# Optimization experiments

Measured on AMD Instinct MI355X. Metric: run time of the kernel, lower is better.

Reference implementation:

```python
import jax, jax.numpy as jnp
import numpy as np
from jax import lax

EPS = 1e-5
DN = ('NCHW', 'OIHW', 'NCHW')

def _sign(v):
    # (v >= 0) * 2 - 1
    return jnp.where(v >= 0, 1.0, -1.0).astype(v.dtype)

def _conv(x, w, b):
    y = lax.conv_general_dilated(x, w, (1, 1), 'VALID', dimension_numbers=DN)
    return y + b[None, :, None, None]

def _bn(x):
    # BatchNorm2d(affine=False), training mode: biased batch stats over (N,H,W)
    m = jnp.mean(x, axis=(0, 2, 3), keepdims=True)
    v = jnp.var(x, axis=(0, 2, 3), keepdims=True)
    return (x - m) * lax.rsqrt(v + EPS)

def setup_inputs() -> dict:
    key = jax.random.key(0)
    ks = jax.random.split(key, 9)
    f = jnp.float32
    B = 8192
    x = jax.random.normal(ks[0], (B, 1, 28, 28), dtype=f)
    # conv params, clipped to [-1, 1] as in clip_weights()
    w1 = jnp.clip(jax.random.normal(ks[1], (32, 1, 9, 9), dtype=f) * 0.1, -1, 1)
    b1 = jnp.clip(jax.random.normal(ks[2], (32,), dtype=f) * 0.1, -1, 1)
    w2 = jnp.clip(jax.random.normal(ks[3], (16, 32, 9, 9), dtype=f) * 0.1, -1, 1)
    b2 = jnp.clip(jax.random.normal(ks[4], (16,), dtype=f) * 0.1, -1, 1)
    w3 = jnp.clip(jax.random.normal(ks[5], (8, 16, 9, 9), dtype=f) * 0.1, -1, 1)
    b3 = jnp.clip(jax.random.normal(ks[6], (8,), dtype=f) * 0.1, -1, 1)
    wl = jnp.clip(jax.random.normal(ks[7], (10, 8, 4, 4), dtype=f) * 0.1, -1, 1)
    bl = jnp.clip(jax.random.normal(ks[8], (10,), dtype=f) * 0.1, -1, 1)
    return {"x": x, "w1": w1, "b1": b1, "w2": w2, "b2": b2,
            "w3": w3, "b3": b3, "wl": wl, "bl": bl}

def _block(x, w, b, act=True, norm=True, binarized=True):
    if binarized:
        w, b = _sign(w), _sign(b)
    x = _conv(x, w, b)
    if norm:
        x = _bn(x)
    if act:
        x = _sign(x) if binarized else jax.nn.relu(x)
    return x

def reference(x, w1, b1, w2, b2, w3, b3, wl, bl):
    x = _sign(x)                        # binarize input activations
    x = _block(x, w1, b1)               # (B, 32, 20, 20)
    x = _block(x, w2, b2)               # (B, 16, 12, 12)
    x = _block(x, w3, b3)               # (B,  8,  4,  4)
    x = _block(x, wl, bl, act=False, norm=False)  # (B, 10, 1, 1), binarized weights
    return x.reshape(-1, 10)
```

## Files before the change

### kernel.cpp

```cpp
#include <hip/hip_runtime.h>
#include <stdint.h>

#define BATCH 8192

#define OFF_W1R3   0
#define OFF_W2P    384
#define OFF_W3P    6144
#define OFF_WLB    9600
#define OFF_SBL    9760
#define OFF_TTOT   9856
#define OFF_S3     10184
#define OFF_S2PART 10496
#define OFF_Z2     76800
#define OFF_Z3     37825792

__global__ __launch_bounds__(256) void k1_pack_tsum(const float* __restrict__ x,
                                                    const float* __restrict__ w1,
                                                    const float* __restrict__ w2,
                                                    const float* __restrict__ w3,
                                                    const float* __restrict__ wl,
                                                    const float* __restrict__ bl,
                                                    uint8_t* __restrict__ ws) {
  int* Ttot = (int*)(ws + OFF_TTOT);
  const int tid = threadIdx.x;

  if (blockIdx.x == 0) {
    uint32_t* W1R3 = (uint32_t*)(ws + OFF_W1R3);
    uint32_t* W2P  = (uint32_t*)(ws + OFF_W2P);
    uint32_t* W3P  = (uint32_t*)(ws + OFF_W3P);
    uint64_t* WLB  = (uint64_t*)(ws + OFF_WLB);
    float*    SBL  = (float*)(ws + OFF_SBL);
    for (int e = tid; e < 96; e += 256) {
      int oc = e / 3, i = e % 3;
      uint32_t m = 0;
      for (int rr = 0; rr < 3; ++rr)
        for (int kw = 0; kw < 9; ++kw)
          if (w1[oc*81 + (3*i+rr)*9 + kw] < 0.f) m |= 1u << (rr*9 + kw);
      W1R3[e] = m;
    }
    for (int e = tid; e < 648; e += 256) {
      int och = e / 81, k = e % 81;
      int kh = k / 9, kw = k % 9;
      uint32_t m0 = 0, m1 = 0;
      int oc0 = och*2;
      for (int ic = 0; ic < 32; ++ic) {
        if (w2[(oc0*32 + ic)*81 + k] < 0.f)     m0 |= 1u << ic;
        if (w2[((oc0+1)*32 + ic)*81 + k] < 0.f) m1 |= 1u << ic;
      }
      int idx = ((och*9 + kh)*10 + kw)*2;
      W2P[idx] = m0; W2P[idx+1] = m1;
    }
    for (int e = tid; e < 72; e += 256) {
      int idx = (e*10 + 9)*2;
      W2P[idx] = 0; W2P[idx+1] = 0;
    }
    for (int e = tid; e < 648; e += 256) {
      int oc = e / 81, k = e % 81;
      int kh = k / 9, kw = k % 9;
      uint32_t m = 0;
      for (int ic = 0; ic < 16; ++ic)
        if (w3[(oc*16 + ic)*81 + k] < 0.f) m |= 1u << ic;
      W3P[(oc*9 + kh)*12 + kw] = m;
    }
    for (int e = tid; e < 216; e += 256) {
      int row = e / 3, p = e % 3;
      W3P[row*12 + 9 + p] = 0;
    }
    for (int e = tid; e < 20; e += 256) {
      int oc = e >> 1, word = e & 1;
      uint64_t m = 0;
      for (int b = 0; b < 64; ++b)
        if (wl[oc*128 + word*64 + b] < 0.f) m |= 1ull << b;
      WLB[e] = m;
    }
    if (tid < 10) SBL[tid] = (bl[tid] >= 0.f) ? 1.f : -1.f;
  }

  __shared__ uint32_t rowm[896];
  __shared__ int Tacc[81];
  if (tid < 81) Tacc[tid] = 0;
  __syncthreads();

  const int img0 = blockIdx.x * 32;
  #pragma unroll
  for (int it = 0; it < 4; ++it) {
    int R = tid + it*256;
    if (R < 896) {
      int il = R / 28, r = R % 28;
      const float4* xr = (const float4*)(x + (size_t)(img0 + il) * 784 + r * 28);
      uint32_t m = 0;
      #pragma unroll
      for (int j = 0; j < 7; ++j) {
        float4 v = xr[j];
        if (v.x < 0.f) m |= 1u << (j*4+0);
        if (v.y < 0.f) m |= 1u << (j*4+1);
        if (v.z < 0.f) m |= 1u << (j*4+2);
        if (v.w < 0.f) m |= 1u << (j*4+3);
      }
      rowm[R] = m;
    }
  }
  __syncthreads();

  for (int T = tid; T < 288; T += 256) {
    int il = T / 9, kw = T % 9;
    int base = il * 28;
    int n9[9];
    int sum20 = 0;
    #pragma unroll
    for (int r = 0; r < 20; ++r) {
      int n = __popc((rowm[base + r] >> kw) & 0xFFFFFu);
      if (r < 9) n9[r] = n;
      sum20 += n;
    }
    atomicAdd(&Tacc[kw], 400 - 2*sum20);
    #pragma unroll
    for (int kh = 1; kh <= 8; ++kh) {
      int nadd = __popc((rowm[base + kh + 19] >> kw) & 0xFFFFFu);
      sum20 += nadd - n9[kh-1];
      atomicAdd(&Tacc[kh*9 + kw], 400 - 2*sum20);
    }
  }
  __syncthreads();
  if (tid < 81) atomicAdd(&Ttot[tid], Tacc[tid]);
}

#define K2_IMGS 8
__global__ __launch_bounds__(256) void k2_conv12(const float* __restrict__ x,
                                                 uint8_t* __restrict__ ws) {
  const uint32_t* W1R3g = (const uint32_t*)(ws + OFF_W1R3);
  const uint32_t* W2Pg  = (const uint32_t*)(ws + OFF_W2P);
  const int* Ttot = (const int*)(ws + OFF_TTOT);
  int* S2P = (int*)(ws + OFF_S2PART);

  __shared__ uint32_t __attribute__((aligned(16))) rowm[K2_IMGS*28];
  __shared__ uint32_t __attribute__((aligned(16))) w1r3[96];
  __shared__ uint32_t __attribute__((aligned(16))) w2p[1440];
  __shared__ int tlds[81];
  __shared__ int t1s[32];
  __shared__ uint32_t __attribute__((aligned(16))) A1s[K2_IMGS*400];
  __shared__ int s2acc[16];

  const int tid = threadIdx.x;
  const int img0 = blockIdx.x * K2_IMGS;

  for (int e = tid; e < 96; e += 256)   w1r3[e] = W1R3g[e];
  for (int e = tid; e < 1440; e += 256) w2p[e]  = W2Pg[e];
  if (tid < 81) tlds[tid] = Ttot[tid];
  if (tid < 16) s2acc[tid] = 0;
  if (tid < K2_IMGS*28) {
    int il = tid / 28, rr = tid % 28;
    const float4* xr = (const float4*)(x + (size_t)(img0 + il) * 784 + rr * 28);
    uint32_t m = 0;
    #pragma unroll
    for (int j = 0; j < 7; ++j) {
      float4 v = xr[j];
      if (v.x < 0.f) m |= 1u << (j*4+0);
      if (v.y < 0.f) m |= 1u << (j*4+1);
      if (v.z < 0.f) m |= 1u << (j*4+2);
      if (v.w < 0.f) m |= 1u << (j*4+3);
    }
    rowm[tid] = m;
  }
  __syncthreads();

  if (tid < 32) {
    long long S = 0;
    for (int kh = 0; kh < 9; ++kh)
      for (int kw = 0; kw < 9; ++kw) {
        int bit = (w1r3[tid*3 + kh/3] >> ((kh%3)*9 + kw)) & 1;
        S += (long long)(1 - 2*bit) * tlds[kh*9 + kw];
      }
    const long long N1 = (long long)BATCH * 400;
    long long q = S / N1, rr = S % N1;
    long long t = q + (rr > 0 ? 1 : 0);
    if ((t & 1) == 0) t += 1;
    t1s[tid] = (int)t;
  }
  __syncthreads();

  for (int G = tid; G < K2_IMGS*80; G += 256) {
    int il = G / 80, rem = G - il*80;
    int oh = rem >> 2, ow0 = (rem & 3) * 5;
    uint32_t R[9];
    #pragma unroll
    for (int i = 0; i < 9; ++i) R[i] = rowm[il*28 + oh + i];
    uint32_t win[5][3];
    #pragma unroll
    for (int j = 0; j < 5; ++j) {
      int ow = ow0 + j;
      #pragma unroll
      for (int i = 0; i < 3; ++i) {
        uint32_t b0 = (R[3*i]   >> ow) & 0x1FFu;
        uint32_t b1 = (R[3*i+1] >> ow) & 0x1FFu;
        uint32_t b2 = (R[3*i+2] >> ow) & 0x1FFu;
        win[j][i] = b0 | (b1 << 9) | (b2 << 18);
      }
    }
    uint32_t mask[5] = {0,0,0,0,0};
    #pragma unroll
    for (int ocg = 0; ocg < 4; ++ocg) {
      const uint4* wp = (const uint4*)&w1r3[ocg*24];
      uint32_t wr[24];
      #pragma unroll
      for (int q = 0; q < 6; ++q) {
        uint4 v = wp[q];
        wr[q*4+0]=v.x; wr[q*4+1]=v.y; wr[q*4+2]=v.z; wr[q*4+3]=v.w;
      }
      #pragma unroll
      for (int o8 = 0; o8 < 8; ++o8) {
        int oc = ocg*8 + o8;
        int t = t1s[oc];
        #pragma unroll
        for (int j = 0; j < 5; ++j) {
          int mm = __popc(win[j][0] ^ wr[o8*3])
                 + __popc(win[j][1] ^ wr[o8*3+1])
                 + __popc(win[j][2] ^ wr[o8*3+2]);
          mask[j] |= (uint32_t)((81 - 2*mm) < t) << oc;
        }
      }
    }
    #pragma unroll
    for (int j = 0; j < 5; ++j) A1s[il*400 + oh*20 + ow0 + j] = mask[j];
  }
  __syncthreads();

  uint32_t* Z2w = (uint32_t*)(ws + OFF_Z2);
  const int och = tid & 7, oc0 = och << 1;
  int sl0 = 0, sl1 = 0;
  for (int r = 0; r < 3; ++r) {
    int G = tid + r*256;
    int il = G / 96, rem = G - il*96;
    int oy = rem >> 3;
    const uint32_t* A = &A1s[il*400 + oy*20];
    int acc0[12], acc1[12];
    #pragma unroll
    for (int p = 0; p < 12; ++p) { acc0[p] = 0; acc1[p] = 0; }
    for (int kh = 0; kh < 9; ++kh) {
      const uint4* ar = (const uint4*)(A + kh*20);
      uint32_t a[20];
      #pragma unroll
      for (int q = 0; q < 5; ++q) {
        uint4 v = ar[q];
        a[q*4+0]=v.x; a[q*4+1]=v.y; a[q*4+2]=v.z; a[q*4+3]=v.w;
      }
      const uint4* wp4 = (const uint4*)&w2p[(och*9 + kh)*20];
      uint32_t wbuf[20];
      #pragma unroll
      for (int q = 0; q < 5; ++q) {
        uint4 v = wp4[q];
        wbuf[q*4+0]=v.x; wbuf[q*4+1]=v.y; wbuf[q*4+2]=v.z; wbuf[q*4+3]=v.w;
      }
      #pragma unroll
      for (int kw = 0; kw < 9; ++kw) {
        uint32_t w0 = wbuf[2*kw], w1v = wbuf[2*kw+1];
        #pragma unroll
        for (int px = 0; px < 12; ++px) {
          acc0[px] += __popc(a[kw+px] ^ w0);
          acc1[px] += __popc(a[kw+px] ^ w1v);
        }
      }
    }
    size_t wbase = (size_t)(img0+il)*1152 + (size_t)oy*96 + och;
    #pragma unroll
    for (int px = 0; px < 12; ++px) {
      int z0 = 2592 - 2*acc0[px], z1v = 2592 - 2*acc1[px];
      sl0 += z0; sl1 += z1v;
      Z2w[wbase + px*8] = (uint32_t)(uint16_t)(int16_t)z0
                        | ((uint32_t)(uint16_t)(int16_t)z1v << 16);
    }
  }
  atomicAdd(&s2acc[oc0],   sl0);
  atomicAdd(&s2acc[oc0+1], sl1);
  __syncthreads();
  if (tid < 16) S2P[blockIdx.x*16 + tid] = s2acc[tid];
}

__global__ __launch_bounds__(256) void k3_conv3(uint8_t* __restrict__ ws) {
  const int* S2P = (const int*)(ws + OFF_S2PART);
  const uint32_t* W3Pg = (const uint32_t*)(ws + OFF_W3P);
  const uint32_t* Z2w = (const uint32_t*)(ws + OFF_Z2);
  uint32_t* Z3w = (uint32_t*)(ws + OFF_Z3);
  unsigned long long* S3 = (unsigned long long*)(ws + OFF_S3);

  __shared__ uint32_t __attribute__((aligned(16))) w3p[864];
  __shared__ int part[256];
  __shared__ int t2s[16];
  __shared__ uint32_t __attribute__((aligned(16))) A2[32*144];
  __shared__ int s3acc[8];

  const int tid = threadIdx.x;
  const int img0 = blockIdx.x * 32;

  {
    int c = tid & 15, g = tid >> 4;
    int s = 0;
    for (int j = 0; j < 64; ++j) s += S2P[(g + 16*j)*16 + c];
    part[tid] = s;
  }
  for (int e = tid; e < 864; e += 256) w3p[e] = W3Pg[e];
  if (tid < 8) s3acc[tid] = 0;
  __syncthreads();
  if (tid < 16) {
    long long S = 0;
    #pragma unroll
    for (int g = 0; g < 16; ++g) S += (long long)part[g*16 + tid];
    const long long N2 = (long long)BATCH * 144;
    long long q = S / N2, r = S % N2;
    long long t = q + (r > 0 ? 1 : 0);
    if (t & 1) t += 1;
    t2s[tid] = (int)t;
  }
  __syncthreads();

  #pragma unroll
  for (int j = 0; j < 18; ++j) {
    int idx = tid + j*256;
    const uint4* zp = (const uint4*)&Z2w[(size_t)(img0 + idx/144)*1152 + (size_t)(idx%144)*8];
    uint4 v0 = zp[0], v1 = zp[1];
    uint32_t zz[8] = {v0.x,v0.y,v0.z,v0.w, v1.x,v1.y,v1.z,v1.w};
    uint32_t m = 0;
    #pragma unroll
    for (int i = 0; i < 8; ++i) {
      int zlo = (int)(short)(zz[i] & 0xFFFFu);
      int zhi = (int)zz[i] >> 16;
      m |= (uint32_t)(zlo < t2s[2*i])   << (2*i);
      m |= (uint32_t)(zhi < t2s[2*i+1]) << (2*i+1);
    }
    A2[idx] = m;
  }
  __syncthreads();

  const int il = tid >> 3, oc = tid & 7;
  int acc[16];
  #pragma unroll
  for (int i = 0; i < 16; ++i) acc[i] = 0;
  #pragma unroll
  for (int r = 0; r < 12; ++r) {
    const uint4* ar = (const uint4*)&A2[il*144 + r*12];
    uint4 v0 = ar[0], v1 = ar[1], v2 = ar[2];
    uint32_t a[12] = {v0.x,v0.y,v0.z,v0.w, v1.x,v1.y,v1.z,v1.w, v2.x,v2.y,v2.z,v2.w};
    #pragma unroll
    for (int oy = 0; oy < 4; ++oy) {
      if (r - oy >= 0 && r - oy <= 8) {
        int kh = r - oy;
        const uint4* wr = (const uint4*)&w3p[(oc*9 + kh)*12];
        uint4 w0 = wr[0], w1v = wr[1], w2v = wr[2];
        uint32_t w[9] = {w0.x,w0.y,w0.z,w0.w, w1v.x,w1v.y,w1v.z,w1v.w, w2v.x};
        #pragma unroll
        for (int ox = 0; ox < 4; ++ox) {
          int m = 0;
          #pragma unroll
          for (int kw = 0; kw < 9; ++kw) m += __popc(a[ox+kw] ^ w[kw]);
          acc[oy*4+ox] += m;
        }
      }
    }
  }
  int ssum = 0;
  uint32_t packed[8];
  #pragma unroll
  for (int h = 0; h < 8; ++h) {
    int za = 1296 - 2*acc[2*h], zb = 1296 - 2*acc[2*h+1];
    ssum += za + zb;
    packed[h] = (uint32_t)(uint16_t)(int16_t)za | ((uint32_t)(uint16_t)(int16_t)zb << 16);
  }
  uint4* zp = (uint4*)&Z3w[(size_t)(img0 + il)*64 + oc*8];
  zp[0] = make_uint4(packed[0], packed[1], packed[2], packed[3]);
  zp[1] = make_uint4(packed[4], packed[5], packed[6], packed[7]);
  atomicAdd(&s3acc[oc], ssum);
  __syncthreads();
  if (tid < 8)
    atomicAdd(&S3[tid], (unsigned long long)(long long)s3acc[tid]);
}

__global__ __launch_bounds__(256) void k4_final(uint8_t* __restrict__ ws,
                                                float* __restrict__ out) {
  const uint32_t* Z3w = (const uint32_t*)(ws + OFF_Z3);
  const long long* S3 = (const long long*)(ws + OFF_S3);
  const uint64_t* WLBg = (const uint64_t*)(ws + OFF_WLB);
  const float* SBLg = (const float*)(ws + OFF_SBL);
  __shared__ int t3[8];
  __shared__ uint64_t wlb[20];
  __shared__ float sbl[10];
  const int tid = threadIdx.x;
  if (tid < 8) {
    long long S = S3[tid];
    const long long N3 = (long long)BATCH * 16;
    long long q = S / N3, r = S % N3;
    long long t = q + (r > 0 ? 1 : 0);
    if (t & 1) t += 1;
    t3[tid] = (int)t;
  }
  if (tid < 20) wlb[tid] = WLBg[tid];
  if (tid < 10) sbl[tid] = SBLg[tid];
  __syncthreads();
  int img = blockIdx.x * 256 + tid;
  const uint4* zp = (const uint4*)&Z3w[(size_t)img * 64];
  uint32_t zz[64];
  #pragma unroll
  for (int q = 0; q < 16; ++q) {
    uint4 v = zp[q];
    zz[q*4+0]=v.x; zz[q*4+1]=v.y; zz[q*4+2]=v.z; zz[q*4+3]=v.w;
  }
  uint64_t a0 = 0, a1 = 0;
  #pragma unroll
  for (int j = 0; j < 64; ++j) {
    int z = (j & 1) ? ((int)zz[j>>1] >> 16) : (int)(short)(zz[j>>1] & 0xFFFFu);
    a0 |= (uint64_t)(z < t3[j >> 4]) << j;
  }
  #pragma unroll
  for (int j = 0; j < 64; ++j) {
    int z = (j & 1) ? ((int)zz[32 + (j>>1)] >> 16) : (int)(short)(zz[32 + (j>>1)] & 0xFFFFu);
    a1 |= (uint64_t)(z < t3[(64 + j) >> 4]) << j;
  }
  #pragma unroll
  for (int oc = 0; oc < 10; ++oc) {
    int mism = __popcll(a0 ^ wlb[oc*2]) + __popcll(a1 ^ wlb[oc*2 + 1]);
    out[(size_t)img*10 + oc] = (float)(128 - 2*mism) + sbl[oc];
  }
}

extern "C" void kernel_launch(void* const* d_in, const int* in_sizes, int n_in,
                              void* d_out, int out_size, void* d_ws, size_t ws_size,
                              hipStream_t stream) {
  (void)in_sizes; (void)n_in; (void)out_size; (void)ws_size;
  const float* x  = (const float*)d_in[0];
  const float* w1 = (const float*)d_in[1];
  const float* w2 = (const float*)d_in[3];
  const float* w3 = (const float*)d_in[5];
  const float* wl = (const float*)d_in[7];
  const float* bl = (const float*)d_in[8];
  uint8_t* ws = (uint8_t*)d_ws;
  float* out = (float*)d_out;

  hipMemsetAsync(ws + OFF_TTOT, 0, 400, stream);
  k1_pack_tsum<<<256, 256, 0, stream>>>(x, w1, w2, w3, wl, bl, ws);
  k2_conv12<<<1024, 256, 0, stream>>>(x, ws);
  k3_conv3<<<256, 256, 0, stream>>>(ws);
  k4_final<<<32, 256, 0, stream>>>(ws, out);
}
```

Before: 267.8 us.

## Restructure conv2 to one output channel per thread and halve per-block work

The conv2 stage now gives each thread a single output channel instead of a pair. This cuts the accumulator and weight registers, stores fp16-sized halfwords directly, and repacks the conv2 weights per channel with 12-word padded rows. Blocks handle 4 images instead of 8, with twice as many blocks and a launch-bounds occupancy hint. k1 and k4 are also split into more, smaller blocks. The conv1 threshold is precomputed as a popcount bound, and the conv2 partial sums are folded into 256 atomically-accumulated slots that are zeroed by the memset. In exchange, the halfword stores are narrower and weight staging per block is more redundant.

New measurement: 310.6 us. 1.16x slower.

```diff
diff --git a/kernel.cpp b/kernel.cpp
--- a/kernel.cpp
+++ b/kernel.cpp
@@ -5,12 +5,12 @@
 
 #define OFF_W1R3   0
 #define OFF_W2P    384
-#define OFF_W3P    6144
-#define OFF_WLB    9600
-#define OFF_SBL    9760
-#define OFF_TTOT   9856
-#define OFF_S3     10184
-#define OFF_S2PART 10496
+#define OFF_W3P    7296
+#define OFF_WLB    10752
+#define OFF_SBL    10912
+#define OFF_TTOT   10960
+#define OFF_S3     11288
+#define OFF_S2PART 11360
 #define OFF_Z2     76800
 #define OFF_Z3     37825792
 
@@ -38,21 +38,17 @@
           if (w1[oc*81 + (3*i+rr)*9 + kw] < 0.f) m |= 1u << (rr*9 + kw);
       W1R3[e] = m;
     }
-    for (int e = tid; e < 648; e += 256) {
-      int och = e / 81, k = e % 81;
+    for (int e = tid; e < 1296; e += 256) {
+      int oc = e / 81, k = e % 81;
       int kh = k / 9, kw = k % 9;
-      uint32_t m0 = 0, m1 = 0;
-      int oc0 = och*2;
-      for (int ic = 0; ic < 32; ++ic) {
-        if (w2[(oc0*32 + ic)*81 + k] < 0.f)     m0 |= 1u << ic;
-        if (w2[((oc0+1)*32 + ic)*81 + k] < 0.f) m1 |= 1u << ic;
-      }
-      int idx = ((och*9 + kh)*10 + kw)*2;
-      W2P[idx] = m0; W2P[idx+1] = m1;
-    }
-    for (int e = tid; e < 72; e += 256) {
-      int idx = (e*10 + 9)*2;
-      W2P[idx] = 0; W2P[idx+1] = 0;
+      uint32_t m = 0;
+      for (int ic = 0; ic < 32; ++ic)
+        if (w2[(oc*32 + ic)*81 + k] < 0.f) m |= 1u << ic;
+      W2P[(oc*9 + kh)*12 + kw] = m;
+    }
+    for (int e = tid; e < 432; e += 256) {
+      int row = e / 3, p = e % 3;
+      W2P[row*12 + 9 + p] = 0;
     }
     for (int e = tid; e < 648; e += 256) {
       int oc = e / 81, k = e % 81;
@@ -76,16 +72,16 @@
     if (tid < 10) SBL[tid] = (bl[tid] >= 0.f) ? 1.f : -1.f;
   }
 
-  __shared__ uint32_t rowm[896];
+  __shared__ uint32_t rowm[448];
   __shared__ int Tacc[81];
   if (tid < 81) Tacc[tid] = 0;
   __syncthreads();
 
-  const int img0 = blockIdx.x * 32;
-  #pragma unroll
-  for (int it = 0; it < 4; ++it) {
+  const int img0 = blockIdx.x * 16;
+  #pragma unroll
+  for (int it = 0; it < 2; ++it) {
     int R = tid + it*256;
-    if (R < 896) {
+    if (R < 448) {
       int il = R / 28, r = R % 28;
       const float4* xr = (const float4*)(x + (size_t)(img0 + il) * 784 + r * 28);
       uint32_t m = 0;
@@ -102,7 +98,7 @@
   }
   __syncthreads();
 
-  for (int T = tid; T < 288; T += 256) {
+  for (int T = tid; T < 144; T += 256) {
     int il = T / 9, kw = T % 9;
     int base = il * 28;
     int n9[9];
@@ -125,9 +121,9 @@
   if (tid < 81) atomicAdd(&Ttot[tid], Tacc[tid]);
 }
 
-#define K2_IMGS 8
-__global__ __launch_bounds__(256) void k2_conv12(const float* __restrict__ x,
-                                                 uint8_t* __restrict__ ws) {
+#define K2_IMGS 4
+__global__ __launch_bounds__(256, 5) void k2_conv12(const float* __restrict__ x,
+                                                    uint8_t* __restrict__ ws) {
   const uint32_t* W1R3g = (const uint32_t*)(ws + OFF_W1R3);
   const uint32_t* W2Pg  = (const uint32_t*)(ws + OFF_W2P);
   const int* Ttot = (const int*)(ws + OFF_TTOT);
@@ -135,7 +131,7 @@
 
   __shared__ uint32_t __attribute__((aligned(16))) rowm[K2_IMGS*28];
   __shared__ uint32_t __attribute__((aligned(16))) w1r3[96];
-  __shared__ uint32_t __attribute__((aligned(16))) w2p[1440];
+  __shared__ uint32_t __attribute__((aligned(16))) w2p[1728];
   __shared__ int tlds[81];
   __shared__ int t1s[32];
   __shared__ uint32_t __attribute__((aligned(16))) A1s[K2_IMGS*400];
@@ -145,7 +141,7 @@
   const int img0 = blockIdx.x * K2_IMGS;
 
   for (int e = tid; e < 96; e += 256)   w1r3[e] = W1R3g[e];
-  for (int e = tid; e < 1440; e += 256) w2p[e]  = W2Pg[e];
+  for (int e = tid; e < 1728; e += 256) w2p[e]  = W2Pg[e];
   if (tid < 81) tlds[tid] = Ttot[tid];
   if (tid < 16) s2acc[tid] = 0;
   if (tid < K2_IMGS*28) {
@@ -175,7 +171,7 @@
     long long q = S / N1, rr = S % N1;
     long long t = q + (rr > 0 ? 1 : 0);
     if ((t & 1) == 0) t += 1;
-    t1s[tid] = (int)t;
+    t1s[tid] = (int)((81 - t) / 2);
   }
   __syncthreads();
 
@@ -210,13 +206,13 @@
       #pragma unroll
       for (int o8 = 0; o8 < 8; ++o8) {
         int oc = ocg*8 + o8;
-        int t = t1s[oc];
+        int thr = t1s[oc];
         #pragma unroll
         for (int j = 0; j < 5; ++j) {
           int mm = __popc(win[j][0] ^ wr[o8*3])
                  + __popc(win[j][1] ^ wr[o8*3+1])
                  + __popc(win[j][2] ^ wr[o8*3+2]);
-          mask[j] |= (uint32_t)((81 - 2*mm) < t) << oc;
+          mask[j] |= (uint32_t)(mm > thr) << oc;
         }
       }
     }
@@ -225,55 +221,48 @@
   }
   __syncthreads();
 
-  uint32_t* Z2w = (uint32_t*)(ws + OFF_Z2);
-  const int och = tid & 7, oc0 = och << 1;
-  int sl0 = 0, sl1 = 0;
+  unsigned short* Z2h = (unsigned short*)(ws + OFF_Z2);
+  const int oc = tid & 15;
+  const uint32_t* W = &w2p[oc*108];
+  int sl = 0;
   for (int r = 0; r < 3; ++r) {
-    int G = tid + r*256;
-    int il = G / 96, rem = G - il*96;
-    int oy = rem >> 3;
+    const int G = tid + r*256;
+    const int grp = G >> 4;
+    const int il = grp / 12, oy = grp - il*12;
     const uint32_t* A = &A1s[il*400 + oy*20];
-    int acc0[12], acc1[12];
-    #pragma unroll
-    for (int p = 0; p < 12; ++p) { acc0[p] = 0; acc1[p] = 0; }
+    int acc[12];
+    #pragma unroll
+    for (int p = 0; p < 12; ++p) acc[p] = 0;
+    #pragma unroll
     for (int kh = 0; kh < 9; ++kh) {
       const uint4* ar = (const uint4*)(A + kh*20);
-      uint32_t a[20];
-      #pragma unroll
-      for (int q = 0; q < 5; ++q) {
-        uint4 v = ar[q];
-        a[q*4+0]=v.x; a[q*4+1]=v.y; a[q*4+2]=v.z; a[q*4+3]=v.w;
-      }
-      const uint4* wp4 = (const uint4*)&w2p[(och*9 + kh)*20];
-      uint32_t wbuf[20];
-      #pragma unroll
-      for (int q = 0; q < 5; ++q) {
-        uint4 v = wp4[q];
-        wbuf[q*4+0]=v.x; wbuf[q*4+1]=v.y; wbuf[q*4+2]=v.z; wbuf[q*4+3]=v.w;
-      }
+      uint4 v0 = ar[0], v1 = ar[1], v2 = ar[2], v3 = ar[3], v4 = ar[4];
+      uint32_t a[20] = {v0.x,v0.y,v0.z,v0.w, v1.x,v1.y,v1.z,v1.w,
+                        v2.x,v2.y,v2.z,v2.w, v3.x,v3.y,v3.z,v3.w,
+                        v4.x,v4.y,v4.z,v4.w};
+      const uint4* wr4 = (const uint4*)(W + kh*12);
+      uint4 w0 = wr4[0], w1v = wr4[1], w2v = wr4[2];
+      uint32_t w[9] = {w0.x,w0.y,w0.z,w0.w, w1v.x,w1v.y,w1v.z,w1v.w, w2v.x};
       #pragma unroll
       for (int kw = 0; kw < 9; ++kw) {
-        uint32_t w0 = wbuf[2*kw], w1v = wbuf[2*kw+1];
         #pragma unroll
-        for (int px = 0; px < 12; ++px) {
-          acc0[px] += __popc(a[kw+px] ^ w0);
-          acc1[px] += __popc(a[kw+px] ^ w1v);
-        }
-      }
-    }
-    size_t wbase = (size_t)(img0+il)*1152 + (size_t)oy*96 + och;
+        for (int px = 0; px < 12; ++px)
+          acc[px] += __popc(a[kw+px] ^ w[kw]);
+      }
+    }
+    size_t base = (size_t)(img0+il)*2304 + (size_t)(oy*192) + oc;
+    int s = 0;
     #pragma unroll
     for (int px = 0; px < 12; ++px) {
-      int z0 = 2592 - 2*acc0[px], z1v = 2592 - 2*acc1[px];
-      sl0 += z0; sl1 += z1v;
-      Z2w[wbase + px*8] = (uint32_t)(uint16_t)(int16_t)z0
-                        | ((uint32_t)(uint16_t)(int16_t)z1v << 16);
-    }
-  }
-  atomicAdd(&s2acc[oc0],   sl0);
-  atomicAdd(&s2acc[oc0+1], sl1);
-  __syncthreads();
-  if (tid < 16) S2P[blockIdx.x*16 + tid] = s2acc[tid];
+      int z = 2592 - 2*acc[px];
+      s += z;
+      Z2h[base + px*16] = (unsigned short)(short)z;
+    }
+    sl += s;
+  }
+  atomicAdd(&s2acc[oc], sl);
+  __syncthreads();
+  if (tid < 16) atomicAdd(&S2P[(blockIdx.x & 255)*16 + tid], s2acc[tid]);
 }
 
 __global__ __launch_bounds__(256) void k3_conv3(uint8_t* __restrict__ ws) {
@@ -295,7 +284,7 @@
   {
     int c = tid & 15, g = tid >> 4;
     int s = 0;
-    for (int j = 0; j < 64; ++j) s += S2P[(g + 16*j)*16 + c];
+    for (int j = 0; j < 16; ++j) s += S2P[(g + 16*j)*16 + c];
     part[tid] = s;
   }
   for (int e = tid; e < 864; e += 256) w3p[e] = W3Pg[e];
@@ -374,8 +363,8 @@
     atomicAdd(&S3[tid], (unsigned long long)(long long)s3acc[tid]);
 }
 
-__global__ __launch_bounds__(256) void k4_final(uint8_t* __restrict__ ws,
-                                                float* __restrict__ out) {
+__global__ __launch_bounds__(64) void k4_final(uint8_t* __restrict__ ws,
+                                               float* __restrict__ out) {
   const uint32_t* Z3w = (const uint32_t*)(ws + OFF_Z3);
   const long long* S3 = (const long long*)(ws + OFF_S3);
   const uint64_t* WLBg = (const uint64_t*)(ws + OFF_WLB);
@@ -395,7 +384,7 @@
   if (tid < 20) wlb[tid] = WLBg[tid];
   if (tid < 10) sbl[tid] = SBLg[tid];
   __syncthreads();
-  int img = blockIdx.x * 256 + tid;
+  int img = blockIdx.x * 64 + tid;
   const uint4* zp = (const uint4*)&Z3w[(size_t)img * 64];
   uint32_t zz[64];
   #pragma unroll
@@ -434,9 +423,9 @@
   uint8_t* ws = (uint8_t*)d_ws;
   float* out = (float*)d_out;
 
-  hipMemsetAsync(ws + OFF_TTOT, 0, 400, stream);
-  k1_pack_tsum<<<256, 256, 0, stream>>>(x, w1, w2, w3, wl, bl, ws);
-  k2_conv12<<<1024, 256, 0, stream>>>(x, ws);
+  hipMemsetAsync(ws + OFF_TTOT, 0, OFF_S2PART + 256*16*4 - OFF_TTOT, stream);
+  k1_pack_tsum<<<512, 256, 0, stream>>>(x, w1, w2, w3, wl, bl, ws);
+  k2_conv12<<<2048, 256, 0, stream>>>(x, ws);
   k3_conv3<<<256, 256, 0, stream>>>(ws);
-  k4_final<<<32, 256, 0, stream>>>(ws, out);
+  k4_final<<<128, 64, 0, stream>>>(ws, out);
 }
```
